# Optimization experiments

Hardware: AMD Instinct MI355X
Metric: run time of the kernel (lower is better)

## Reference

```python
import jax, jax.numpy as jnp
import numpy as np

DIM = 256
RES = 64
HEADS = 8
WS = 8            # window_size
CS = (8, 64)      # cross_size (cs1 == W so cross grid broadcasts against window grid)
HEAD_DIM = DIM // HEADS
SCALE = HEAD_DIM ** -0.5


def _partition(x, B, sh, sw):
    # x: [B, L, C] -> [B*heads, H//sh, W//sw, sh*sw, head_dim]
    H = W = RES
    C = DIM
    x = x.reshape(B, H // sh, sh, W // sw, sw, HEADS, HEAD_DIM)
    x = x.transpose(0, 5, 1, 3, 2, 4, 6)
    return x.reshape(B * HEADS, H // sh, W // sw, sh * sw, HEAD_DIM)


def setup_inputs() -> dict:
    key = jax.random.key(0)
    qkv = jax.random.normal(key, (3, 8, RES * RES, DIM), dtype=jnp.float32)
    return {"qkv": qkv}


def reference(qkv) -> jnp.ndarray:
    q, k, v = qkv[0], qkv[1], qkv[2]
    B, L, C = q.shape
    H = W = RES

    qw = _partition(q, B, WS, WS) * SCALE            # [Bh, H/ws, W/ws, ws*ws, hd]
    kc = _partition(k, B, CS[0], CS[1])              # [Bh, H/cs0, 1, cs0*cs1, hd]
    vc = _partition(v, B, CS[0], CS[1])

    # Original einsum 'bhwnc,bqkmc->bhwnm' sums k over its cross-window grid (q,k axes);
    # equivalently pre-sum k over those axes, then contract over head_dim.
    k_sum = kc.sum(axis=(1, 2))                      # [Bh, m, hd]
    attn = jnp.einsum('bhwnc,bmc->bhwnm', qw, k_sum) # [Bh, H/ws, W/ws, n, m]
    attn = jax.nn.softmax(attn, axis=-1)

    # broadcast matmul: vc's cross grid (H/cs0, 1) broadcasts to (H/ws, W/ws)
    x = attn @ vc                                    # [Bh, H/ws, W/ws, n, hd]

    x = x.reshape(B, HEADS, H // WS, W // WS, WS, WS, HEAD_DIM)
    x = x.transpose(0, 2, 4, 3, 5, 1, 6).reshape(B, H, W, C).reshape(B, -1, C)
    return x
```

## Files before the change

### kernel.cpp

```cpp
#include <hip/hip_runtime.h>
#include <hip/hip_bf16.h>

#define NB 8
#define L_TOT 4096
#define DIM 256
#define HEADS 8
#define HEAD_DIM 32
#define M_TOT 512
#define QSCALE (0.17677669529663687f * 1.4426950408889634f)

typedef float f32x16 __attribute__((ext_vector_type(16)));
typedef short bf16x8 __attribute__((ext_vector_type(8)));

union BF8 { bf16x8 v; unsigned u[4]; uint2 u2[2]; };

__device__ __forceinline__ unsigned cvt2(float lo, float hi) {
    __hip_bfloat162 h = __float22bfloat162_rn(make_float2(lo, hi));
    union { __hip_bfloat162 h2; unsigned u; } un;
    un.h2 = h;
    return un.u;
}

__global__ __launch_bounds__(256) void ksum_kernel(const float* __restrict__ k,
                                                   unsigned short* __restrict__ ks) {
    const int blk = blockIdx.x;
    const int bh = blk >> 4, part = blk & 15;
    const int b = bh >> 3, head = bh & 7;
    const float* kb = k + (size_t)b * L_TOT * DIM + head * HEAD_DIM;
    const int c0 = (threadIdx.x & 7) * 4;
    const int m = part * 32 + (threadIdx.x >> 3);
    float4 s = make_float4(0.f, 0.f, 0.f, 0.f);
#pragma unroll
    for (int hq = 0; hq < 8; ++hq) {
        const float4 f = *(const float4*)(kb + (size_t)(hq * 512 + m) * DIM + c0);
        s.x += f.x; s.y += f.y; s.z += f.z; s.w += f.w;
    }
    uint2 o;
    o.x = cvt2(s.x, s.y);
    o.y = cvt2(s.z, s.w);
    *(uint2*)(ks + ((size_t)bh * M_TOT + m) * HEAD_DIM + c0) = o;
}

template <bool USE_WS>
__global__ __launch_bounds__(512, 4) void attn_kernel(const float* __restrict__ q,
                                                      const float* __restrict__ kg,
                                                      const float* __restrict__ v,
                                                      const unsigned short* __restrict__ ks,
                                                      float* __restrict__ out) {
    constexpr int VT_SH = 32 * 516;
    constexpr int INV_SH = 8 * 32 * 2;
    __shared__ unsigned short smem[USE_WS ? (VT_SH + INV_SH) : (VT_SH + INV_SH + 512 * 36)];
    unsigned short* vT = smem;

    const int tid = threadIdx.x;
    const int wave = tid >> 6;
    const int lane = tid & 63;
    const int ql = lane & 31;
    const int hi = lane >> 5;

    const int bid = blockIdx.x;
    const int wk = (bid & 7) * 128 + (bid >> 3);
    const int bh = wk >> 4, h = (wk >> 1) & 7, half = wk & 1;
    const int b = bh >> 3, head = bh & 7;

    const float* vbase = v + ((size_t)b * L_TOT + h * M_TOT) * DIM + head * HEAD_DIM;

#pragma unroll
    for (int it = 0; it < 8; ++it) {
        const int idx = it * 512 + tid;
        const int m = idx >> 3, c0 = (idx & 7) * 4;
        const float4 f = *(const float4*)(vbase + (size_t)m * DIM + c0);
        const unsigned w0 = cvt2(f.x, f.y), w1 = cvt2(f.z, f.w);
        vT[(c0 + 0) * 516 + m] = (unsigned short)w0;
        vT[(c0 + 1) * 516 + m] = (unsigned short)(w0 >> 16);
        vT[(c0 + 2) * 516 + m] = (unsigned short)w1;
        vT[(c0 + 3) * 516 + m] = (unsigned short)(w1 >> 16);
    }
    unsigned short* KS = smem + VT_SH + INV_SH;
    if (!USE_WS) {
        const float* kb = kg + (size_t)b * L_TOT * DIM + head * HEAD_DIM;
        for (int idx = tid; idx < M_TOT * HEAD_DIM; idx += 512) {
            const int m = idx >> 5, c = idx & 31;
            float s = 0.f;
#pragma unroll
            for (int hq = 0; hq < 8; ++hq)
                s += kb[(size_t)(hq * 512 + m) * DIM + c];
            KS[m * 36 + c] = (unsigned short)cvt2(s, 0.f);
        }
    }
    __syncthreads();

    const int g = half * 8 + wave;
    const int wcol = g >> 1, n0 = (g & 1) * 32;
    const int n = n0 + ql;
    const int Lq = (h * 8 + (n >> 3)) * 64 + wcol * 8 + (n & 7);
    const float* qp = q + ((size_t)b * L_TOT + Lq) * DIM + head * HEAD_DIM;

    BF8 qf0, qf1;
    {
        const float4 f0 = *(const float4*)(qp + 8 * hi);
        const float4 f1 = *(const float4*)(qp + 8 * hi + 4);
        qf0.u[0] = cvt2(f0.x * QSCALE, f0.y * QSCALE);
        qf0.u[1] = cvt2(f0.z * QSCALE, f0.w * QSCALE);
        qf0.u[2] = cvt2(f1.x * QSCALE, f1.y * QSCALE);
        qf0.u[3] = cvt2(f1.z * QSCALE, f1.w * QSCALE);
        const float4 f2 = *(const float4*)(qp + 16 + 8 * hi);
        const float4 f3 = *(const float4*)(qp + 16 + 8 * hi + 4);
        qf1.u[0] = cvt2(f2.x * QSCALE, f2.y * QSCALE);
        qf1.u[1] = cvt2(f2.z * QSCALE, f2.w * QSCALE);
        qf1.u[2] = cvt2(f3.x * QSCALE, f3.y * QSCALE);
        qf1.u[3] = cvt2(f3.z * QSCALE, f3.w * QSCALE);
    }

    const unsigned short* ksb = ks + (size_t)bh * (M_TOT * HEAD_DIM);
    const unsigned short* vb0 = vT + ql * 516 + 8 * hi;
    float* invW = (float*)(smem + VT_SH) + wave * 32;

    f32x16 O;
#pragma unroll
    for (int r = 0; r < 16; ++r) O[r] = 0.f;
    float lsum = 0.f;

    BF8 a0, a1, b0, b1;
    if (USE_WS) {
        a0.v = *(const bf16x8*)(ksb + (size_t)ql * 32 + 8 * hi);
        a1.v = *(const bf16x8*)(ksb + (size_t)ql * 32 + 16 + 8 * hi);
    }

    auto body = [&](int M0, BF8& c0, BF8& c1, BF8& p0, BF8& p1, int M0n) {
        if (USE_WS) {
            p0.v = *(const bf16x8*)(ksb + (size_t)(M0n + ql) * 32 + 8 * hi);
            p1.v = *(const bf16x8*)(ksb + (size_t)(M0n + ql) * 32 + 16 + 8 * hi);
        } else {
            const unsigned short* kr = KS + (M0 + ql) * 36 + 8 * hi;
            c0.u2[0] = *(const uint2*)(kr);
            c0.u2[1] = *(const uint2*)(kr + 4);
            c1.u2[0] = *(const uint2*)(kr + 16);
            c1.u2[1] = *(const uint2*)(kr + 20);
        }
        f32x16 S;
#pragma unroll
        for (int r = 0; r < 16; ++r) S[r] = 0.f;
        S = __builtin_amdgcn_mfma_f32_32x32x16_bf16(c0.v, qf0.v, S, 0, 0, 0);
        S = __builtin_amdgcn_mfma_f32_32x32x16_bf16(c1.v, qf1.v, S, 0, 0, 0);

        BF8 VB0, VB1;
        const unsigned short* vb = vb0 + M0;
        VB0.u2[0] = *(const uint2*)(vb);
        VB0.u2[1] = *(const uint2*)(vb + 4);
        VB1.u2[0] = *(const uint2*)(vb + 16);
        VB1.u2[1] = *(const uint2*)(vb + 20);

        float p[16];
#pragma unroll
        for (int r = 0; r < 16; ++r) p[r] = __builtin_amdgcn_exp2f(S[r]);
#pragma unroll
        for (int r = 0; r < 16; ++r) lsum += p[r];

        unsigned w0 = cvt2(p[0], p[1]),   w1 = cvt2(p[2], p[3]);
        unsigned w2 = cvt2(p[4], p[5]),   w3 = cvt2(p[6], p[7]);
        unsigned w4 = cvt2(p[8], p[9]),   w5 = cvt2(p[10], p[11]);
        unsigned w6 = cvt2(p[12], p[13]), w7 = cvt2(p[14], p[15]);
        asm("v_permlane32_swap_b32 %0, %1" : "+v"(w0), "+v"(w2));
        asm("v_permlane32_swap_b32 %0, %1" : "+v"(w1), "+v"(w3));
        asm("v_permlane32_swap_b32 %0, %1" : "+v"(w4), "+v"(w6));
        asm("v_permlane32_swap_b32 %0, %1" : "+v"(w5), "+v"(w7));
        BF8 PA0, PA1;
        PA0.u[0] = w0; PA0.u[1] = w1; PA0.u[2] = w2; PA0.u[3] = w3;
        PA1.u[0] = w4; PA1.u[1] = w5; PA1.u[2] = w6; PA1.u[3] = w7;
        O = __builtin_amdgcn_mfma_f32_32x32x16_bf16(PA0.v, VB0.v, O, 0, 0, 0);
        O = __builtin_amdgcn_mfma_f32_32x32x16_bf16(PA1.v, VB1.v, O, 0, 0, 0);
    };

    for (int i = 0; i < 8; ++i) {
        const int M0 = i * 64;
        body(M0,      a0, a1, b0, b1, M0 + 32);
        body(M0 + 32, b0, b1, a0, a1, (M0 + 64) & 511);
    }

    lsum += __shfl_xor(lsum, 32, 64);
    const float inv = __builtin_amdgcn_rcpf(lsum);
    if (hi == 0) invW[ql] = inv;

    const int rowBase = h * 512 + (n0 >> 3) * 64 + wcol * 8 + 4 * hi;
    float* ob = out + ((size_t)b * L_TOT + rowBase) * DIM + head * HEAD_DIM + ql;
#pragma unroll
    for (int t = 0; t < 4; ++t) {
        const float4 iv = *(const float4*)(invW + 8 * t + 4 * hi);
        ob[(size_t)(t * 64 + 0) * DIM] = O[4 * t + 0] * iv.x;
        ob[(size_t)(t * 64 + 1) * DIM] = O[4 * t + 1] * iv.y;
        ob[(size_t)(t * 64 + 2) * DIM] = O[4 * t + 2] * iv.z;
        ob[(size_t)(t * 64 + 3) * DIM] = O[4 * t + 3] * iv.w;
    }
}

extern "C" void kernel_launch(void* const* d_in, const int* in_sizes, int n_in,
                              void* d_out, int out_size, void* d_ws, size_t ws_size,
                              hipStream_t stream) {
    const float* qkv = (const float*)d_in[0];
    const float* q = qkv;
    const float* k = qkv + (size_t)NB * L_TOT * DIM;
    const float* v = qkv + (size_t)2 * NB * L_TOT * DIM;
    float* out = (float*)d_out;
    const size_t ks_bytes = (size_t)NB * HEADS * M_TOT * HEAD_DIM * 2;
    if (ws_size >= ks_bytes) {
        unsigned short* ks = (unsigned short*)d_ws;
        ksum_kernel<<<dim3(1024), dim3(256), 0, stream>>>(k, ks);
        attn_kernel<true><<<dim3(1024), dim3(512), 0, stream>>>(q, k, v, ks, out);
    } else {
        attn_kernel<false><<<dim3(1024), dim3(512), 0, stream>>>(q, k, v, nullptr, out);
    }
}
```

Before: 175.0 us.

## Stage pre-swizzled K-sum and V fragments in LDS, halve grid with two query groups

Result: no change. 174.2 us (-0.5%).

```diff
diff --git a/kernel.cpp b/kernel.cpp
--- a/kernel.cpp
+++ b/kernel.cpp
@@ -12,7 +12,7 @@
 typedef float f32x16 __attribute__((ext_vector_type(16)));
 typedef short bf16x8 __attribute__((ext_vector_type(8)));
 
-union BF8 { bf16x8 v; unsigned u[4]; uint2 u2[2]; };
+union BF8 { bf16x8 v; unsigned u[4]; uint2 u2[2]; uint4 u4; };
 
 __device__ __forceinline__ unsigned cvt2(float lo, float hi) {
     __hip_bfloat162 h = __float22bfloat162_rn(make_float2(lo, hi));
@@ -38,7 +38,10 @@
     uint2 o;
     o.x = cvt2(s.x, s.y);
     o.y = cvt2(s.z, s.w);
-    *(uint2*)(ks + ((size_t)bh * M_TOT + m) * HEAD_DIM + c0) = o;
+    const int lane = (m & 31) + 32 * ((c0 >> 3) & 1);
+    const size_t off = (size_t)bh * 16384 + (size_t)(m >> 5) * 1024 +
+                       (c0 >= 16 ? 512 : 0) + lane * 8 + (c0 & 7);
+    *(uint2*)(ks + off) = o;
 }
 
 template <bool USE_WS>
@@ -47,10 +50,11 @@
                                                       const float* __restrict__ v,
                                                       const unsigned short* __restrict__ ks,
                                                       float* __restrict__ out) {
-    constexpr int VT_SH = 32 * 516;
-    constexpr int INV_SH = 8 * 32 * 2;
-    __shared__ unsigned short smem[USE_WS ? (VT_SH + INV_SH) : (VT_SH + INV_SH + 512 * 36)];
-    unsigned short* vT = smem;
+    constexpr int KSF_OFF = 16384;
+    constexpr int INV_OFF = 32768;
+    __shared__ unsigned short smem[33280];
+    unsigned short* vF = smem;
+    unsigned short* ksF = smem + KSF_OFF;
 
     const int tid = threadIdx.x;
     const int wave = tid >> 6;
@@ -59,138 +63,144 @@
     const int hi = lane >> 5;
 
     const int bid = blockIdx.x;
-    const int wk = (bid & 7) * 128 + (bid >> 3);
-    const int bh = wk >> 4, h = (wk >> 1) & 7, half = wk & 1;
+    const int wk = (bid & 7) * 64 + (bid >> 3);
+    const int bh = wk >> 3, h = wk & 7;
     const int b = bh >> 3, head = bh & 7;
 
+    if (USE_WS) {
+        const uint4* ksrc4 = (const uint4*)(ks + (size_t)bh * 16384);
+        uint4* kdst4 = (uint4*)ksF;
+        const uint4 t0 = ksrc4[tid], t1 = ksrc4[512 + tid];
+        const uint4 t2 = ksrc4[1024 + tid], t3 = ksrc4[1536 + tid];
+        kdst4[tid] = t0; kdst4[512 + tid] = t1;
+        kdst4[1024 + tid] = t2; kdst4[1536 + tid] = t3;
+    } else {
+        const float* kb = kg + (size_t)b * L_TOT * DIM + head * HEAD_DIM;
+#pragma unroll
+        for (int it = 0; it < 8; ++it) {
+            const int idx = it * 512 + tid;
+            const int m = idx >> 3, c0 = (idx & 7) * 4;
+            float4 s = make_float4(0.f, 0.f, 0.f, 0.f);
+#pragma unroll
+            for (int hq = 0; hq < 8; ++hq) {
+                const float4 f = *(const float4*)(kb + (size_t)(hq * 512 + m) * DIM + c0);
+                s.x += f.x; s.y += f.y; s.z += f.z; s.w += f.w;
+            }
+            uint2 o; o.x = cvt2(s.x, s.y); o.y = cvt2(s.z, s.w);
+            const int ln = (m & 31) + 32 * ((c0 >> 3) & 1);
+            *(uint2*)(ksF + (m >> 5) * 1024 + (c0 >= 16 ? 512 : 0) + ln * 8 + (c0 & 7)) = o;
+        }
+    }
+
     const float* vbase = v + ((size_t)b * L_TOT + h * M_TOT) * DIM + head * HEAD_DIM;
-
 #pragma unroll
     for (int it = 0; it < 8; ++it) {
         const int idx = it * 512 + tid;
         const int m = idx >> 3, c0 = (idx & 7) * 4;
         const float4 f = *(const float4*)(vbase + (size_t)m * DIM + c0);
         const unsigned w0 = cvt2(f.x, f.y), w1 = cvt2(f.z, f.w);
-        vT[(c0 + 0) * 516 + m] = (unsigned short)w0;
-        vT[(c0 + 1) * 516 + m] = (unsigned short)(w0 >> 16);
-        vT[(c0 + 2) * 516 + m] = (unsigned short)w1;
-        vT[(c0 + 3) * 516 + m] = (unsigned short)(w1 >> 16);
-    }
-    unsigned short* KS = smem + VT_SH + INV_SH;
-    if (!USE_WS) {
-        const float* kb = kg + (size_t)b * L_TOT * DIM + head * HEAD_DIM;
-        for (int idx = tid; idx < M_TOT * HEAD_DIM; idx += 512) {
-            const int m = idx >> 5, c = idx & 31;
-            float s = 0.f;
-#pragma unroll
-            for (int hq = 0; hq < 8; ++hq)
-                s += kb[(size_t)(hq * 512 + m) * DIM + c];
-            KS[m * 36 + c] = (unsigned short)cvt2(s, 0.f);
-        }
+        unsigned short* bp = vF + (m >> 5) * 1024 + ((m >> 4) & 1) * 512 +
+                             (c0 + 32 * ((m >> 3) & 1)) * 8 + (m & 7);
+        bp[0]  = (unsigned short)w0;
+        bp[8]  = (unsigned short)(w0 >> 16);
+        bp[16] = (unsigned short)w1;
+        bp[24] = (unsigned short)(w1 >> 16);
     }
     __syncthreads();
 
-    const int g = half * 8 + wave;
-    const int wcol = g >> 1, n0 = (g & 1) * 32;
-    const int n = n0 + ql;
-    const int Lq = (h * 8 + (n >> 3)) * 64 + wcol * 8 + (n & 7);
-    const float* qp = q + ((size_t)b * L_TOT + Lq) * DIM + head * HEAD_DIM;
-
-    BF8 qf0, qf1;
-    {
-        const float4 f0 = *(const float4*)(qp + 8 * hi);
-        const float4 f1 = *(const float4*)(qp + 8 * hi + 4);
-        qf0.u[0] = cvt2(f0.x * QSCALE, f0.y * QSCALE);
-        qf0.u[1] = cvt2(f0.z * QSCALE, f0.w * QSCALE);
-        qf0.u[2] = cvt2(f1.x * QSCALE, f1.y * QSCALE);
-        qf0.u[3] = cvt2(f1.z * QSCALE, f1.w * QSCALE);
-        const float4 f2 = *(const float4*)(qp + 16 + 8 * hi);
-        const float4 f3 = *(const float4*)(qp + 16 + 8 * hi + 4);
-        qf1.u[0] = cvt2(f2.x * QSCALE, f2.y * QSCALE);
-        qf1.u[1] = cvt2(f2.z * QSCALE, f2.w * QSCALE);
-        qf1.u[2] = cvt2(f3.x * QSCALE, f3.y * QSCALE);
-        qf1.u[3] = cvt2(f3.z * QSCALE, f3.w * QSCALE);
-    }
-
-    const unsigned short* ksb = ks + (size_t)bh * (M_TOT * HEAD_DIM);
-    const unsigned short* vb0 = vT + ql * 516 + 8 * hi;
-    float* invW = (float*)(smem + VT_SH) + wave * 32;
-
-    f32x16 O;
-#pragma unroll
-    for (int r = 0; r < 16; ++r) O[r] = 0.f;
-    float lsum = 0.f;
-
-    BF8 a0, a1, b0, b1;
-    if (USE_WS) {
-        a0.v = *(const bf16x8*)(ksb + (size_t)ql * 32 + 8 * hi);
-        a1.v = *(const bf16x8*)(ksb + (size_t)ql * 32 + 16 + 8 * hi);
-    }
-
-    auto body = [&](int M0, BF8& c0, BF8& c1, BF8& p0, BF8& p1, int M0n) {
-        if (USE_WS) {
-            p0.v = *(const bf16x8*)(ksb + (size_t)(M0n + ql) * 32 + 8 * hi);
-            p1.v = *(const bf16x8*)(ksb + (size_t)(M0n + ql) * 32 + 16 + 8 * hi);
-        } else {
-            const unsigned short* kr = KS + (M0 + ql) * 36 + 8 * hi;
-            c0.u2[0] = *(const uint2*)(kr);
-            c0.u2[1] = *(const uint2*)(kr + 4);
-            c1.u2[0] = *(const uint2*)(kr + 16);
-            c1.u2[1] = *(const uint2*)(kr + 20);
-        }
-        f32x16 S;
-#pragma unroll
-        for (int r = 0; r < 16; ++r) S[r] = 0.f;
-        S = __builtin_amdgcn_mfma_f32_32x32x16_bf16(c0.v, qf0.v, S, 0, 0, 0);
-        S = __builtin_amdgcn_mfma_f32_32x32x16_bf16(c1.v, qf1.v, S, 0, 0, 0);
-
-        BF8 VB0, VB1;
-        const unsigned short* vb = vb0 + M0;
-        VB0.u2[0] = *(const uint2*)(vb);
-        VB0.u2[1] = *(const uint2*)(vb + 4);
-        VB1.u2[0] = *(const uint2*)(vb + 16);
-        VB1.u2[1] = *(const uint2*)(vb + 20);
-
-        float p[16];
-#pragma unroll
-        for (int r = 0; r < 16; ++r) p[r] = __builtin_amdgcn_exp2f(S[r]);
-#pragma unroll
-        for (int r = 0; r < 16; ++r) lsum += p[r];
-
-        unsigned w0 = cvt2(p[0], p[1]),   w1 = cvt2(p[2], p[3]);
-        unsigned w2 = cvt2(p[4], p[5]),   w3 = cvt2(p[6], p[7]);
-        unsigned w4 = cvt2(p[8], p[9]),   w5 = cvt2(p[10], p[11]);
-        unsigned w6 = cvt2(p[12], p[13]), w7 = cvt2(p[14], p[15]);
-        asm("v_permlane32_swap_b32 %0, %1" : "+v"(w0), "+v"(w2));
-        asm("v_permlane32_swap_b32 %0, %1" : "+v"(w1), "+v"(w3));
-        asm("v_permlane32_swap_b32 %0, %1" : "+v"(w4), "+v"(w6));
-        asm("v_permlane32_swap_b32 %0, %1" : "+v"(w5), "+v"(w7));
-        BF8 PA0, PA1;
-        PA0.u[0] = w0; PA0.u[1] = w1; PA0.u[2] = w2; PA0.u[3] = w3;
-        PA1.u[0] = w4; PA1.u[1] = w5; PA1.u[2] = w6; PA1.u[3] = w7;
-        O = __builtin_amdgcn_mfma_f32_32x32x16_bf16(PA0.v, VB0.v, O, 0, 0, 0);
-        O = __builtin_amdgcn_mfma_f32_32x32x16_bf16(PA1.v, VB1.v, O, 0, 0, 0);
-    };
-
-    for (int i = 0; i < 8; ++i) {
-        const int M0 = i * 64;
-        body(M0,      a0, a1, b0, b1, M0 + 32);
-        body(M0 + 32, b0, b1, a0, a1, (M0 + 64) & 511);
-    }
-
-    lsum += __shfl_xor(lsum, 32, 64);
-    const float inv = __builtin_amdgcn_rcpf(lsum);
-    if (hi == 0) invW[ql] = inv;
-
-    const int rowBase = h * 512 + (n0 >> 3) * 64 + wcol * 8 + 4 * hi;
-    float* ob = out + ((size_t)b * L_TOT + rowBase) * DIM + head * HEAD_DIM + ql;
-#pragma unroll
-    for (int t = 0; t < 4; ++t) {
-        const float4 iv = *(const float4*)(invW + 8 * t + 4 * hi);
-        ob[(size_t)(t * 64 + 0) * DIM] = O[4 * t + 0] * iv.x;
-        ob[(size_t)(t * 64 + 1) * DIM] = O[4 * t + 1] * iv.y;
-        ob[(size_t)(t * 64 + 2) * DIM] = O[4 * t + 2] * iv.z;
-        ob[(size_t)(t * 64 + 3) * DIM] = O[4 * t + 3] * iv.w;
+    const unsigned short* ksW = ksF + lane * 8;
+    const unsigned short* vfW = vF + lane * 8;
+    float* invW = (float*)(smem + INV_OFF) + wave * 32;
+    const float* qbase = q + (size_t)b * L_TOT * DIM + head * HEAD_DIM;
+
+    for (int gi = 0; gi < 2; ++gi) {
+        const int wcol = wave, n0 = gi * 32;
+        const int n = n0 + ql;
+        const int Lq = (h * 8 + (n >> 3)) * 64 + wcol * 8 + (n & 7);
+        const float* qp = qbase + (size_t)Lq * DIM;
+
+        BF8 qf0, qf1;
+        {
+            const float4 f0 = *(const float4*)(qp + 8 * hi);
+            const float4 f1 = *(const float4*)(qp + 8 * hi + 4);
+            qf0.u[0] = cvt2(f0.x * QSCALE, f0.y * QSCALE);
+            qf0.u[1] = cvt2(f0.z * QSCALE, f0.w * QSCALE);
+            qf0.u[2] = cvt2(f1.x * QSCALE, f1.y * QSCALE);
+            qf0.u[3] = cvt2(f1.z * QSCALE, f1.w * QSCALE);
+            const float4 f2 = *(const float4*)(qp + 16 + 8 * hi);
+            const float4 f3 = *(const float4*)(qp + 16 + 8 * hi + 4);
+            qf1.u[0] = cvt2(f2.x * QSCALE, f2.y * QSCALE);
+            qf1.u[1] = cvt2(f2.z * QSCALE, f2.w * QSCALE);
+            qf1.u[2] = cvt2(f3.x * QSCALE, f3.y * QSCALE);
+            qf1.u[3] = cvt2(f3.z * QSCALE, f3.w * QSCALE);
+        }
+
+        f32x16 O;
+#pragma unroll
+        for (int r = 0; r < 16; ++r) O[r] = 0.f;
+        float lsum = 0.f;
+
+        auto qk = [&](int ch) -> f32x16 {
+            BF8 A0, A1;
+            A0.u4 = *(const uint4*)(ksW + ch * 1024);
+            A1.u4 = *(const uint4*)(ksW + ch * 1024 + 512);
+            f32x16 z;
+#pragma unroll
+            for (int r = 0; r < 16; ++r) z[r] = 0.f;
+            f32x16 S = __builtin_amdgcn_mfma_f32_32x32x16_bf16(A0.v, qf0.v, z, 0, 0, 0);
+            return __builtin_amdgcn_mfma_f32_32x32x16_bf16(A1.v, qf1.v, S, 0, 0, 0);
+        };
+
+        auto smPV = [&](const f32x16& S, int ch) {
+            BF8 VB0, VB1;
+            VB0.u4 = *(const uint4*)(vfW + ch * 1024);
+            VB1.u4 = *(const uint4*)(vfW + ch * 1024 + 512);
+            float p[16];
+#pragma unroll
+            for (int r = 0; r < 16; ++r) p[r] = __builtin_amdgcn_exp2f(S[r]);
+            const float s0 = (p[0] + p[1]) + (p[2] + p[3]);
+            const float s1 = (p[4] + p[5]) + (p[6] + p[7]);
+            const float s2 = (p[8] + p[9]) + (p[10] + p[11]);
+            const float s3 = (p[12] + p[13]) + (p[14] + p[15]);
+            lsum += (s0 + s1) + (s2 + s3);
+
+            unsigned w0 = cvt2(p[0], p[1]),   w1 = cvt2(p[2], p[3]);
+            unsigned w2 = cvt2(p[4], p[5]),   w3 = cvt2(p[6], p[7]);
+            unsigned w4 = cvt2(p[8], p[9]),   w5 = cvt2(p[10], p[11]);
+            unsigned w6 = cvt2(p[12], p[13]), w7 = cvt2(p[14], p[15]);
+            asm("v_permlane32_swap_b32 %0, %1" : "+v"(w0), "+v"(w2));
+            asm("v_permlane32_swap_b32 %0, %1" : "+v"(w1), "+v"(w3));
+            asm("v_permlane32_swap_b32 %0, %1" : "+v"(w4), "+v"(w6));
+            asm("v_permlane32_swap_b32 %0, %1" : "+v"(w5), "+v"(w7));
+            BF8 PA0, PA1;
+            PA0.u[0] = w0; PA0.u[1] = w1; PA0.u[2] = w2; PA0.u[3] = w3;
+            PA1.u[0] = w4; PA1.u[1] = w5; PA1.u[2] = w6; PA1.u[3] = w7;
+            O = __builtin_amdgcn_mfma_f32_32x32x16_bf16(PA0.v, VB0.v, O, 0, 0, 0);
+            O = __builtin_amdgcn_mfma_f32_32x32x16_bf16(PA1.v, VB1.v, O, 0, 0, 0);
+        };
+
+        f32x16 Sc = qk(0);
+        for (int ch = 0; ch < 15; ++ch) {
+            f32x16 Sn = qk(ch + 1);
+            smPV(Sc, ch);
+            Sc = Sn;
+        }
+        smPV(Sc, 15);
+
+        lsum += __shfl_xor(lsum, 32, 64);
+        const float inv = __builtin_amdgcn_rcpf(lsum);
+        if (hi == 0) invW[ql] = inv;
+
+        const int rowBase = h * 512 + (n0 >> 3) * 64 + wcol * 8 + 4 * hi;
+        float* ob = out + ((size_t)b * L_TOT + rowBase) * DIM + head * HEAD_DIM + ql;
+#pragma unroll
+        for (int t = 0; t < 4; ++t) {
+            const float4 iv = *(const float4*)(invW + 8 * t + 4 * hi);
+            ob[(size_t)(t * 64 + 0) * DIM] = O[4 * t + 0] * iv.x;
+            ob[(size_t)(t * 64 + 1) * DIM] = O[4 * t + 1] * iv.y;
+            ob[(size_t)(t * 64 + 2) * DIM] = O[4 * t + 2] * iv.z;
+            ob[(size_t)(t * 64 + 3) * DIM] = O[4 * t + 3] * iv.w;
+        }
     }
 }
 
@@ -206,8 +216,8 @@
     if (ws_size >= ks_bytes) {
         unsigned short* ks = (unsigned short*)d_ws;
         ksum_kernel<<<dim3(1024), dim3(256), 0, stream>>>(k, ks);
-        attn_kernel<true><<<dim3(1024), dim3(512), 0, stream>>>(q, k, v, ks, out);
+        attn_kernel<true><<<dim3(512), dim3(512), 0, stream>>>(q, k, v, ks, out);
     } else {
-        attn_kernel<false><<<dim3(1024), dim3(512), 0, stream>>>(q, k, v, nullptr, out);
-    }
-}
+        attn_kernel<false><<<dim3(512), dim3(512), 0, stream>>>(q, k, v, nullptr, out);
+    }
+}
```
